# Performance work log

Hardware: AMD Instinct MI355X
Metric: run time of the kernel (lower is better)

## Reference

```python
import jax, jax.numpy as jnp
import numpy as np

N_BINS = 100
LOWER, UPPER = 0.0, 1.0


def setup_inputs() -> dict:
    key = jax.random.key(0)
    outputs = jax.random.uniform(key, (96, 512, 512), dtype=jnp.float32)
    # bin boundaries, identical to np.linspace(lower - 1e-6, upper, n_bins + 1)
    bounds = jnp.asarray(np.linspace(LOWER - 1e-6, UPPER, N_BINS + 1), dtype=jnp.float32)
    return {"outputs": outputs, "bounds": bounds}


def reference(outputs, bounds):
    """Histogram counts: count[i] = #{x : bounds[i] < x <= bounds[i+1]}.

    Single-pass bucketize + scatter-add, replacing the original per-bin
    mask-and-sum loop with identical math (open-left, closed-right bins).
    """
    n_bins = bounds.shape[0] - 1
    x = outputs.ravel()
    # side='left': smallest i with bounds[i] >= x, i.e. bounds[i-1] < x <= bounds[i]
    bins = jnp.searchsorted(bounds, x, side="left") - 1
    valid = (bins >= 0) & (bins < n_bins)
    bins_c = jnp.where(valid, bins, n_bins)  # route out-of-range to dummy bin
    ones = jnp.where(valid, 1.0, 0.0).astype(outputs.dtype)
    count = jnp.zeros(n_bins + 1, dtype=outputs.dtype).at[bins_c].add(ones)
    return count[:n_bins]
```

## Files before the change

### kernel.cpp

```cpp
#include <hip/hip_runtime.h>

#define N_BINS 100
#define BLOCK 1024
#define GRID 512
#define EPS 1e-3f

__global__ __launch_bounds__(BLOCK) void hist_kernel(const float* __restrict__ x,
                                                     const float* __restrict__ bounds,
                                                     float* __restrict__ out,
                                                     int n) {
    __shared__ float sb[N_BINS + 1];
    __shared__ unsigned int sh[N_BINS][32];

    const int tid = threadIdx.x;
    const int col = tid & 31;

    if (tid < N_BINS + 1) sb[tid] = bounds[tid];
    for (int i = tid; i < N_BINS * 32; i += BLOCK) ((unsigned int*)sh)[i] = 0u;
    __syncthreads();

    const float b0 = sb[0];
    const float bN = sb[N_BINS];
    const float scale = (float)N_BINS / (bN - b0);

    const int n4 = n >> 2;
    const float4* __restrict__ x4 = (const float4*)x;
    const int gstride = GRID * BLOCK;
    const int gtid = blockIdx.x * BLOCK + tid;

    for (int i = gtid; i < n4; i += gstride) {
        float4 v = x4[i];
        float vals[4] = {v.x, v.y, v.z, v.w};
        #pragma unroll
        for (int k = 0; k < 4; ++k) {
            float val = vals[k];
            float f = (val - b0) * scale;
            int g = (int)f;
            float r = f - (float)g;
            if (r > EPS && r < 1.0f - EPS && f > 0.0f && f < (float)N_BINS) {
                atomicAdd(&sh[g][col], 1u);
            } else {
                g = min(max(g, 0), N_BINS - 1);
                while (g > 0 && val <= sb[g]) --g;
                while (g < N_BINS - 1 && val > sb[g + 1]) ++g;
                if (val > b0 && val <= bN) atomicAdd(&sh[g][col], 1u);
            }
        }
    }
    for (int i = (n4 << 2) + gtid; i < n; i += gstride) {
        float val = x[i];
        int g = min(max((int)((val - b0) * scale), 0), N_BINS - 1);
        while (g > 0 && val <= sb[g]) --g;
        while (g < N_BINS - 1 && val > sb[g + 1]) ++g;
        if (val > b0 && val <= bN) atomicAdd(&sh[g][col], 1u);
    }

    __syncthreads();
    if (tid < N_BINS) {
        unsigned int c = 0;
        #pragma unroll
        for (int j = 0; j < 32; ++j) c += sh[tid][(j + tid) & 31];
        atomicAdd(&out[tid], (float)c);
    }
}

extern "C" void kernel_launch(void* const* d_in, const int* in_sizes, int n_in,
                              void* d_out, int out_size, void* d_ws, size_t ws_size,
                              hipStream_t stream) {
    const float* x = (const float*)d_in[0];
    const float* bounds = (const float*)d_in[1];
    float* out = (float*)d_out;
    const int n = in_sizes[0];

    hipMemsetAsync(d_out, 0, out_size * sizeof(float), stream);
    hist_kernel<<<GRID, BLOCK, 0, stream>>>(x, bounds, out, n);
}
```

Baseline: 151.4 us.

## Prefetch next float4 and take a wave-uniform fast path for binning

The grid-stride loop becomes a software-pipelined loop that loads the next float4 before binning the current one, so global-memory latency overlaps with the binning work. The per-element divergent branch is replaced by a wave-level __any test: the whole wave uses the cheap computed bin unless some lane has a value close to a bin boundary, in which case it falls back to the exact search against the bounds. The guard band is narrowed from 1e-3 to 1e-4, so the slow path runs less often, but values that sit near a boundary and fall outside the band are trusted to the computed index, which risks an occasional misbinned value. The fast path also issues an atomic with a zero increment for out-of-range values instead of branching around it.

New measurement: 149.0 us. Within noise of the previous version (-1.6%).

```diff
diff --git a/kernel.cpp b/kernel.cpp
--- a/kernel.cpp
+++ b/kernel.cpp
@@ -3,7 +3,7 @@
 #define N_BINS 100
 #define BLOCK 1024
 #define GRID 512
-#define EPS 1e-3f
+#define EPS 1e-4f
 
 __global__ __launch_bounds__(BLOCK) void hist_kernel(const float* __restrict__ x,
                                                      const float* __restrict__ bounds,
@@ -22,34 +22,58 @@
     const float b0 = sb[0];
     const float bN = sb[N_BINS];
     const float scale = (float)N_BINS / (bN - b0);
+    const float c0 = -b0 * scale;
 
     const int n4 = n >> 2;
     const float4* __restrict__ x4 = (const float4*)x;
     const int gstride = GRID * BLOCK;
-    const int gtid = blockIdx.x * BLOCK + tid;
+    int i = blockIdx.x * BLOCK + tid;
 
-    for (int i = gtid; i < n4; i += gstride) {
+    if (i < n4) {
         float4 v = x4[i];
-        float vals[4] = {v.x, v.y, v.z, v.w};
-        #pragma unroll
-        for (int k = 0; k < 4; ++k) {
-            float val = vals[k];
-            float f = (val - b0) * scale;
-            int g = (int)f;
-            float r = f - (float)g;
-            if (r > EPS && r < 1.0f - EPS && f > 0.0f && f < (float)N_BINS) {
-                atomicAdd(&sh[g][col], 1u);
+        for (;;) {
+            const int inext = i + gstride;
+            const bool more = inext < n4;
+            float4 vn = v;
+            if (more) vn = x4[inext];
+
+            float f0 = fmaf(v.x, scale, c0);
+            float f1 = fmaf(v.y, scale, c0);
+            float f2 = fmaf(v.z, scale, c0);
+            float f3 = fmaf(v.w, scale, c0);
+            bool unc = (fabsf(f0 - rintf(f0)) < EPS) | (fabsf(f1 - rintf(f1)) < EPS) |
+                       (fabsf(f2 - rintf(f2)) < EPS) | (fabsf(f3 - rintf(f3)) < EPS);
+
+            if (__any(unc)) {
+                float vals[4] = {v.x, v.y, v.z, v.w};
+                #pragma unroll
+                for (int k = 0; k < 4; ++k) {
+                    float val = vals[k];
+                    int g = min(max((int)fmaf(val, scale, c0), 0), N_BINS - 1);
+                    while (g > 0 && val <= sb[g]) --g;
+                    while (g < N_BINS - 1 && val > sb[g + 1]) ++g;
+                    if (val > b0 && val <= bN) atomicAdd(&sh[g][col], 1u);
+                }
             } else {
-                g = min(max(g, 0), N_BINS - 1);
-                while (g > 0 && val <= sb[g]) --g;
-                while (g < N_BINS - 1 && val > sb[g + 1]) ++g;
-                if (val > b0 && val <= bN) atomicAdd(&sh[g][col], 1u);
+                float fs[4] = {f0, f1, f2, f3};
+                #pragma unroll
+                for (int k = 0; k < 4; ++k) {
+                    float f = fs[k];
+                    int g = min(max((int)f, 0), N_BINS - 1);
+                    unsigned int inc = (f > 0.0f && f < (float)N_BINS) ? 1u : 0u;
+                    atomicAdd(&sh[g][col], inc);
+                }
             }
+
+            if (!more) break;
+            v = vn;
+            i = inext;
         }
     }
-    for (int i = (n4 << 2) + gtid; i < n; i += gstride) {
-        float val = x[i];
-        int g = min(max((int)((val - b0) * scale), 0), N_BINS - 1);
+
+    for (int t = (n4 << 2) + blockIdx.x * BLOCK + tid; t < n; t += gstride) {
+        float val = x[t];
+        int g = min(max((int)fmaf(val, scale, c0), 0), N_BINS - 1);
         while (g > 0 && val <= sb[g]) --g;
         while (g < N_BINS - 1 && val > sb[g + 1]) ++g;
         if (val > b0 && val <= bN) atomicAdd(&sh[g][col], 1u);
```

## Split histogram into bucketize kernel writing byte bins and a separate counting kernel

Applied to the files above, without the earlier changes.

Breaks the fused histogram into two kernels. The first computes each element's bin index and writes it as one byte to the workspace. The second reads the packed bytes and does shared-memory atomic counting. This separates the branchy bucketize work from the atomic-heavy counting, and also changes block/grid sizes and the fast-path epsilon. In exchange it adds about 25 MB of extra global write plus read traffic and a second launch.

After: 203.5 us. 34.4% more time.

```diff
diff --git a/kernel.cpp b/kernel.cpp
--- a/kernel.cpp
+++ b/kernel.cpp
@@ -1,58 +1,87 @@
 #include <hip/hip_runtime.h>
 
 #define N_BINS 100
-#define BLOCK 1024
-#define GRID 512
-#define EPS 1e-3f
+#define BLOCK 256
+#define GRID 2048
+#define EPS 1e-4f
 
-__global__ __launch_bounds__(BLOCK) void hist_kernel(const float* __restrict__ x,
-                                                     const float* __restrict__ bounds,
-                                                     float* __restrict__ out,
-                                                     int n) {
+__global__ __launch_bounds__(BLOCK) void bin_kernel(const float* __restrict__ x,
+                                                    const float* __restrict__ bounds,
+                                                    unsigned char* __restrict__ binout,
+                                                    int n) {
     __shared__ float sb[N_BINS + 1];
-    __shared__ unsigned int sh[N_BINS][32];
-
     const int tid = threadIdx.x;
-    const int col = tid & 31;
-
     if (tid < N_BINS + 1) sb[tid] = bounds[tid];
-    for (int i = tid; i < N_BINS * 32; i += BLOCK) ((unsigned int*)sh)[i] = 0u;
     __syncthreads();
-
-    const float b0 = sb[0];
-    const float bN = sb[N_BINS];
+    const float b0 = sb[0], bN = sb[N_BINS];
     const float scale = (float)N_BINS / (bN - b0);
+    const float c0 = -b0 * scale;
 
     const int n4 = n >> 2;
     const float4* __restrict__ x4 = (const float4*)x;
+    uchar4* __restrict__ b4 = (uchar4*)binout;
     const int gstride = GRID * BLOCK;
-    const int gtid = blockIdx.x * BLOCK + tid;
 
-    for (int i = gtid; i < n4; i += gstride) {
+    for (int i = blockIdx.x * BLOCK + tid; i < n4; i += gstride) {
         float4 v = x4[i];
         float vals[4] = {v.x, v.y, v.z, v.w};
+        unsigned char bb[4];
         #pragma unroll
         for (int k = 0; k < 4; ++k) {
             float val = vals[k];
-            float f = (val - b0) * scale;
+            float f = fmaf(val, scale, c0);
             int g = (int)f;
             float r = f - (float)g;
-            if (r > EPS && r < 1.0f - EPS && f > 0.0f && f < (float)N_BINS) {
-                atomicAdd(&sh[g][col], 1u);
+            if ((r > EPS) & (r < 1.0f - EPS) & (f > 0.0f) & (f < (float)N_BINS)) {
+                bb[k] = (unsigned char)g;
             } else {
                 g = min(max(g, 0), N_BINS - 1);
                 while (g > 0 && val <= sb[g]) --g;
                 while (g < N_BINS - 1 && val > sb[g + 1]) ++g;
-                if (val > b0 && val <= bN) atomicAdd(&sh[g][col], 1u);
+                bb[k] = (val > b0 && val <= bN) ? (unsigned char)g : (unsigned char)0xFF;
+            }
+        }
+        b4[i] = make_uchar4(bb[0], bb[1], bb[2], bb[3]);
+    }
+    for (int t = (n4 << 2) + blockIdx.x * BLOCK + tid; t < n; t += gstride) {
+        float val = x[t];
+        int g = min(max((int)fmaf(val, scale, c0), 0), N_BINS - 1);
+        while (g > 0 && val <= sb[g]) --g;
+        while (g < N_BINS - 1 && val > sb[g + 1]) ++g;
+        binout[t] = (val > b0 && val <= bN) ? (unsigned char)g : (unsigned char)0xFF;
+    }
+}
+
+__global__ __launch_bounds__(BLOCK) void count_kernel(const unsigned char* __restrict__ bins,
+                                                      float* __restrict__ out, int n) {
+    __shared__ unsigned int sh[N_BINS][32];
+    const int tid = threadIdx.x;
+    const int col = tid & 31;
+    for (int i = tid; i < N_BINS * 32; i += BLOCK) ((unsigned int*)sh)[i] = 0u;
+    __syncthreads();
+
+    const int n16 = n >> 4;
+    const uint4* __restrict__ b16 = (const uint4*)bins;
+    const int gstride = GRID * BLOCK;
+
+    for (int i = blockIdx.x * BLOCK + tid; i < n16; i += gstride) {
+        uint4 w = b16[i];
+        unsigned int ws4[4] = {w.x, w.y, w.z, w.w};
+        #pragma unroll
+        for (int j = 0; j < 4; ++j) {
+            unsigned int u = ws4[j];
+            #pragma unroll
+            for (int s = 0; s < 4; ++s) {
+                unsigned int b = (u >> (8 * s)) & 0xFFu;
+                unsigned int g = (b < N_BINS) ? b : 0u;
+                unsigned int inc = (b < N_BINS) ? 1u : 0u;
+                atomicAdd(&sh[g][col], inc);
             }
         }
     }
-    for (int i = (n4 << 2) + gtid; i < n; i += gstride) {
-        float val = x[i];
-        int g = min(max((int)((val - b0) * scale), 0), N_BINS - 1);
-        while (g > 0 && val <= sb[g]) --g;
-        while (g < N_BINS - 1 && val > sb[g + 1]) ++g;
-        if (val > b0 && val <= bN) atomicAdd(&sh[g][col], 1u);
+    for (int t = (n16 << 4) + blockIdx.x * BLOCK + tid; t < n; t += gstride) {
+        unsigned int b = bins[t];
+        if (b < N_BINS) atomicAdd(&sh[b][col], 1u);
     }
 
     __syncthreads();
@@ -70,8 +99,10 @@
     const float* x = (const float*)d_in[0];
     const float* bounds = (const float*)d_in[1];
     float* out = (float*)d_out;
+    unsigned char* binbuf = (unsigned char*)d_ws;
     const int n = in_sizes[0];
 
     hipMemsetAsync(d_out, 0, out_size * sizeof(float), stream);
-    hist_kernel<<<GRID, BLOCK, 0, stream>>>(x, bounds, out, n);
+    bin_kernel<<<GRID, BLOCK, 0, stream>>>(x, bounds, binbuf, n);
+    count_kernel<<<GRID, BLOCK, 0, stream>>>(binbuf, out, n);
 }
```
